# Performance work log

Hardware: AMD Instinct MI355X
Metric: run time of the kernel (lower is better)

## Reference

```python
import jax, jax.numpy as jnp
import numpy as np

B, D, A, M = 262144, 128, 32, 100


def setup_inputs() -> dict:
    key = jax.random.key(0)
    ks = jax.random.split(key, 8)
    s = 0.05
    return {
        "state": jax.random.normal(ks[0], (B, D), jnp.float32),
        "action": jax.random.normal(ks[1], (B, A), jnp.float32),
        "next_state": jax.random.normal(ks[2], (B, D), jnp.float32),
        "seen": jax.random.normal(ks[3], (M, D), jnp.float32),
        "W1": jax.random.normal(ks[4], (D, D + A), jnp.float32) * s,
        "b1": jnp.zeros((D,), jnp.float32),
        "W2": jax.random.normal(ks[5], (D, D), jnp.float32) * s,
        "b2": jnp.zeros((D,), jnp.float32),
        "Wf": jax.random.normal(ks[6], (D, D), jnp.float32) * s,
        "bf": jnp.zeros((D,), jnp.float32),
    }


def reference(state, action, next_state, seen, W1, b1, W2, b2, Wf, bf):
    # predictor: Linear(D+A -> D) -> ReLU -> Linear(D -> D)   (torch: y = x W^T + b)
    x = jnp.concatenate([state, action], axis=-1)            # [B, D+A]
    h = jax.nn.relu(x @ W1.T + b1)                           # [B, D]
    predicted_next = h @ W2.T + b2                           # [B, D]

    # feature_extractor: Linear(D -> D) -> ReLU
    feat = lambda z: jax.nn.relu(z @ Wf.T + bf)
    features_actual = feat(next_state)                       # [B, D]
    features_pred = feat(predicted_next)                     # [B, D]

    # per-sample MSE prediction error (features_actual detached in original)
    fa_sg = jax.lax.stop_gradient(features_actual)
    pred_error = jnp.mean((features_pred - fa_sg) ** 2, axis=-1)  # [B]

    # 1-NN L2 distance to memory buffer, batched via the ||a-b||^2 expansion
    # (avoids materializing [B, M, D])
    a2 = jnp.sum(features_actual ** 2, axis=-1, keepdims=True)    # [B, 1]
    s2 = jnp.sum(seen ** 2, axis=-1)                              # [M]
    d2 = a2 + s2[None, :] - 2.0 * (features_actual @ seen.T)      # [B, M]
    min_dist = jnp.sqrt(jnp.maximum(jnp.min(d2, axis=-1), 0.0))   # [B]
    novelty = jnp.minimum(1.0, min_dist / 10.0)                   # [B]

    curiosity_reward = pred_error * 0.5 + novelty * 0.5
    return jnp.stack([pred_error, novelty, curiosity_reward])     # [3, B]
```

## Files before the change

kernel.cpp:

```cpp
#include <hip/hip_runtime.h>
#include <hip/hip_bf16.h>
#include <math.h>

#define B_TOT 262144

typedef __attribute__((ext_vector_type(8))) short v8s;
typedef __attribute__((ext_vector_type(4))) float v4f;

#define WS_W1 0
#define WS_W2 20480
#define WS_WF 36864
#define WS_SEEN 53248
#define WS_S2_BYTES 135168

__device__ __forceinline__ unsigned short f2bf(float f) {
  union { float f; unsigned u; } cv; cv.f = f;
  unsigned u = cv.u;
  return (unsigned short)((u + 0x7FFFu + ((u >> 16) & 1u)) >> 16);
}
__device__ __forceinline__ float bf2f(unsigned short h) {
  union { unsigned u; float f; } cv; cv.u = ((unsigned)h) << 16;
  return cv.f;
}
__device__ __forceinline__ unsigned f2bf2(float x, float y) {
  float2 f; f.x = x; f.y = y;
  __hip_bfloat162 h = __float22bfloat162_rn(f);
  union { __hip_bfloat162 h; unsigned u; } cv; cv.h = h;
  return cv.u;
}

__global__ void curiosity_prep(const float* __restrict__ W1, const float* __restrict__ W2,
                               const float* __restrict__ Wf, const float* __restrict__ seen,
                               unsigned short* __restrict__ wsb, float* __restrict__ s2) {
  int bid = blockIdx.x;
  if (bid < 264) {
    int idx = bid * 256 + (int)threadIdx.x;
    if (idx < 20480) {
      int f = idx >> 9, r = idx & 511, L = r >> 3, j = r & 7;
      int t = f / 5, c = f - t * 5;
      int n = t * 16 + (L & 15), k = c * 32 + (L >> 4) * 8 + j;
      wsb[idx] = f2bf(W1[n * 160 + k]);
    } else if (idx < 36864) {
      int e = idx - 20480;
      int f = e >> 9, r = e & 511, L = r >> 3, j = r & 7;
      int t = f >> 2, c = f & 3;
      int n = t * 16 + (L & 15), k = c * 32 + (L >> 4) * 8 + j;
      wsb[idx] = f2bf(W2[n * 128 + k]);
    } else if (idx < 53248) {
      int e = idx - 36864;
      int f = e >> 9, r = e & 511, L = r >> 3, j = r & 7;
      int t = f >> 2, c = f & 3;
      int n = t * 16 + (L & 15), k = c * 32 + (L >> 4) * 8 + j;
      wsb[idx] = f2bf(Wf[n * 128 + k]);
    } else {
      int e = idx - 53248;
      int f = e >> 9, r = e & 511, L = r >> 3, j = r & 7;
      int t = f >> 2, c = f & 3;
      int n = t * 16 + (L & 15), k = c * 32 + (L >> 4) * 8 + j;
      float v = (n < 100) ? seen[n * 128 + k] : 0.f;
      wsb[idx] = f2bf(v);
    }
  } else {
    int wv = (int)threadIdx.x >> 6, lane = (int)threadIdx.x & 63;
    int mm = (bid - 264) * 4 + wv;
    float s;
    if (mm < 100) {
      float v0 = seen[mm * 128 + lane], v1 = seen[mm * 128 + 64 + lane];
      s = v0 * v0 + v1 * v1;
#pragma unroll
      for (int msk = 1; msk < 64; msk <<= 1) s += __shfl_xor(s, msk, 64);
    } else {
      s = 1e30f;
    }
    if (lane == 0) s2[mm] = s;
  }
}

__device__ __forceinline__ v8s cvt_frag(float4 lo, float4 hi) {
  union { v8s v; unsigned u[4]; } r;
  r.u[0] = f2bf2(lo.x, lo.y);
  r.u[1] = f2bf2(lo.z, lo.w);
  r.u[2] = f2bf2(hi.x, hi.y);
  r.u[3] = f2bf2(hi.z, hi.w);
  return r.v;
}

__device__ __forceinline__ v8s read_frag(const unsigned short* buf, int m, int q, int c) {
  return *(const v8s*)(buf + m * 136 + c * 32 + q * 8);
}
__device__ __forceinline__ v8s wfrag(const unsigned short* __restrict__ wsb,
                                     int base, int fragIdx, int lane) {
  return *(const v8s*)(wsb + base + fragIdx * 512 + lane * 8);
}

__global__ __launch_bounds__(256, 3) void curiosity_main(
    const float* __restrict__ state, const float* __restrict__ action,
    const float* __restrict__ next_state,
    const float* __restrict__ b1, const float* __restrict__ b2,
    const float* __restrict__ bfv,
    const unsigned short* __restrict__ wsb, const float* __restrict__ s2g,
    float* __restrict__ out) {
  __shared__ __attribute__((aligned(16))) unsigned short s_int[4][2][2176];
  __shared__ float s_o[3][128];

  const int tid = (int)threadIdx.x;
  const int w = tid >> 6, lane = tid & 63;
  const int m = lane & 15, q = lane >> 4;
  const int rowblk = (int)blockIdx.x * 128 + w * 32;

  unsigned short* buf[2] = { &s_int[w][0][0], &s_int[w][1][0] };

  const float* st0 = state + (size_t)(rowblk + m) * 128 + q * 8;
  const float* st1 = st0 + 16 * 128;
  const float* ac0 = action + (size_t)(rowblk + m) * 32 + q * 8;
  const float* ac1 = ac0 + 16 * 32;
  const float* np0 = next_state + (size_t)(rowblk + m) * 128 + q * 8;
  const float* np1 = np0 + 16 * 128;

  float4 sv[2][4][2], av[2][2];
#pragma unroll
  for (int c = 0; c < 4; ++c) {
    sv[0][c][0] = *(const float4*)(st0 + c * 32);
    sv[0][c][1] = *(const float4*)(st0 + c * 32 + 4);
    sv[1][c][0] = *(const float4*)(st1 + c * 32);
    sv[1][c][1] = *(const float4*)(st1 + c * 32 + 4);
  }
  av[0][0] = *(const float4*)(ac0); av[0][1] = *(const float4*)(ac0 + 4);
  av[1][0] = *(const float4*)(ac1); av[1][1] = *(const float4*)(ac1 + 4);

  float bv1[8], bv2[8], bvf[8];
#pragma unroll
  for (int tg = 0; tg < 8; ++tg) bv1[tg] = b1[tg * 16 + m];
#pragma unroll
  for (int tg = 0; tg < 8; ++tg) bv2[tg] = b2[tg * 16 + m];
#pragma unroll
  for (int tg = 0; tg < 8; ++tg) bvf[tg] = bfv[tg * 16 + m];

  v8s a1[2][5];
#pragma unroll
  for (int c = 0; c < 4; ++c) {
    a1[0][c] = cvt_frag(sv[0][c][0], sv[0][c][1]);
    a1[1][c] = cvt_frag(sv[1][c][0], sv[1][c][1]);
  }
  a1[0][4] = cvt_frag(av[0][0], av[0][1]);
  a1[1][4] = cvt_frag(av[1][0], av[1][1]);

#pragma unroll
  for (int hf = 0; hf < 2; ++hf) {
    v8s bfr[20];
#pragma unroll
    for (int c = 0; c < 5; ++c)
#pragma unroll
      for (int tl = 0; tl < 4; ++tl)
        bfr[c * 4 + tl] = wfrag(wsb, WS_W1, (hf * 4 + tl) * 5 + c, lane);
    v4f acc[2][4] = {};
#pragma unroll
    for (int c = 0; c < 5; ++c)
#pragma unroll
      for (int tl = 0; tl < 4; ++tl) {
        acc[0][tl] = __builtin_amdgcn_mfma_f32_16x16x32_bf16(a1[0][c], bfr[c * 4 + tl], acc[0][tl], 0, 0, 0);
        acc[1][tl] = __builtin_amdgcn_mfma_f32_16x16x32_bf16(a1[1][c], bfr[c * 4 + tl], acc[1][tl], 0, 0, 0);
      }
#pragma unroll
    for (int tl = 0; tl < 4; ++tl) {
      int tg = hf * 4 + tl;
      float bv = bv1[tg];
#pragma unroll
      for (int tt = 0; tt < 2; ++tt)
#pragma unroll
        for (int r = 0; r < 4; r += 2) {
          unsigned p = f2bf2(fmaxf(acc[tt][tl][r] + bv, 0.f),
                             fmaxf(acc[tt][tl][r + 1] + bv, 0.f));
          buf[tt][(q * 4 + r) * 136 + tg * 16 + m] = (unsigned short)p;
          buf[tt][(q * 4 + r + 1) * 136 + tg * 16 + m] = (unsigned short)(p >> 16);
        }
    }
  }

  float4 n0v[4][2], n1v[4][2];
#pragma unroll
  for (int c = 0; c < 4; ++c) {
    n0v[c][0] = *(const float4*)(np0 + c * 32);
    n0v[c][1] = *(const float4*)(np0 + c * 32 + 4);
  }

  v8s af[2][4];
#pragma unroll
  for (int c = 0; c < 4; ++c) {
    af[0][c] = read_frag(buf[0], m, q, c);
    af[1][c] = read_frag(buf[1], m, q, c);
  }
  v8s a3[2][4];
#pragma unroll
  for (int hf = 0; hf < 2; ++hf) {
    if (hf == 1) {
#pragma unroll
      for (int c = 0; c < 4; ++c) a3[0][c] = cvt_frag(n0v[c][0], n0v[c][1]);
#pragma unroll
      for (int c = 0; c < 4; ++c) {
        n1v[c][0] = *(const float4*)(np1 + c * 32);
        n1v[c][1] = *(const float4*)(np1 + c * 32 + 4);
      }
    }
    v8s bfr[16];
#pragma unroll
    for (int c = 0; c < 4; ++c)
#pragma unroll
      for (int tl = 0; tl < 4; ++tl)
        bfr[c * 4 + tl] = wfrag(wsb, WS_W2, (hf * 4 + tl) * 4 + c, lane);
    v4f acc[2][4] = {};
#pragma unroll
    for (int c = 0; c < 4; ++c)
#pragma unroll
      for (int tl = 0; tl < 4; ++tl) {
        acc[0][tl] = __builtin_amdgcn_mfma_f32_16x16x32_bf16(af[0][c], bfr[c * 4 + tl], acc[0][tl], 0, 0, 0);
        acc[1][tl] = __builtin_amdgcn_mfma_f32_16x16x32_bf16(af[1][c], bfr[c * 4 + tl], acc[1][tl], 0, 0, 0);
      }
#pragma unroll
    for (int tl = 0; tl < 4; ++tl) {
      int tg = hf * 4 + tl;
      float bv = bv2[tg];
#pragma unroll
      for (int tt = 0; tt < 2; ++tt)
#pragma unroll
        for (int r = 0; r < 4; r += 2) {
          unsigned p = f2bf2(acc[tt][tl][r] + bv, acc[tt][tl][r + 1] + bv);
          buf[tt][(q * 4 + r) * 136 + tg * 16 + m] = (unsigned short)p;
          buf[tt][(q * 4 + r + 1) * 136 + tg * 16 + m] = (unsigned short)(p >> 16);
        }
    }
  }

  v8s a4[2][4];
#pragma unroll
  for (int c = 0; c < 4; ++c) {
    a4[0][c] = read_frag(buf[0], m, q, c);
    a4[1][c] = read_frag(buf[1], m, q, c);
  }
#pragma unroll
  for (int c = 0; c < 4; ++c) a3[1][c] = cvt_frag(n1v[c][0], n1v[c][1]);

  float s2v[7];
#pragma unroll
  for (int tl = 0; tl < 7; ++tl) s2v[tl] = s2g[tl * 16 + m];

  float pe[2][4] = {};
  float a2s[2][4] = {};
#pragma unroll
  for (int hf = 0; hf < 2; ++hf) {
#pragma unroll
    for (int tl = 0; tl < 4; ++tl) {
      v8s bfr[4];
#pragma unroll
      for (int c = 0; c < 4; ++c)
        bfr[c] = wfrag(wsb, WS_WF, (hf * 4 + tl) * 4 + c, lane);
      v4f fa0 = {}, fa1 = {}, fp0 = {}, fp1 = {};
#pragma unroll
      for (int c = 0; c < 4; ++c) {
        fa0 = __builtin_amdgcn_mfma_f32_16x16x32_bf16(a3[0][c], bfr[c], fa0, 0, 0, 0);
        fa1 = __builtin_amdgcn_mfma_f32_16x16x32_bf16(a3[1][c], bfr[c], fa1, 0, 0, 0);
        fp0 = __builtin_amdgcn_mfma_f32_16x16x32_bf16(a4[0][c], bfr[c], fp0, 0, 0, 0);
        fp1 = __builtin_amdgcn_mfma_f32_16x16x32_bf16(a4[1][c], bfr[c], fp1, 0, 0, 0);
      }
      int tg = hf * 4 + tl;
      float bv = bvf[tg];
#pragma unroll
      for (int tt = 0; tt < 2; ++tt) {
        const v4f& fav = tt ? fa1 : fa0;
        const v4f& fpv = tt ? fp1 : fp0;
#pragma unroll
        for (int rp = 0; rp < 2; ++rp) {
          int r = rp * 2;
          unsigned p = f2bf2(fmaxf(fav[r] + bv, 0.f),
                             fmaxf(fav[r + 1] + bv, 0.f));
          buf[tt][(q * 4 + r) * 136 + tg * 16 + m] = (unsigned short)p;
          buf[tt][(q * 4 + r + 1) * 136 + tg * 16 + m] = (unsigned short)(p >> 16);
          float flo = bf2f((unsigned short)p), fhi = bf2f((unsigned short)(p >> 16));
          a2s[tt][r] += flo * flo;
          a2s[tt][r + 1] += fhi * fhi;
          float d0 = fmaxf(fpv[r] + bv, 0.f) - flo;
          float d1 = fmaxf(fpv[r + 1] + bv, 0.f) - fhi;
          pe[tt][r] += d0 * d0;
          pe[tt][r + 1] += d1 * d1;
        }
      }
    }
  }

#pragma unroll
  for (int tt = 0; tt < 2; ++tt)
#pragma unroll
    for (int r = 0; r < 4; ++r)
#pragma unroll
      for (int msk = 1; msk < 16; msk <<= 1) {
        pe[tt][r] += __shfl_xor(pe[tt][r], msk, 16);
        a2s[tt][r] += __shfl_xor(a2s[tt][r], msk, 16);
      }

  v8s a5[2][4];
#pragma unroll
  for (int c = 0; c < 4; ++c) {
    a5[0][c] = read_frag(buf[0], m, q, c);
    a5[1][c] = read_frag(buf[1], m, q, c);
  }
  float dmin[2][4] = {{3.4e38f, 3.4e38f, 3.4e38f, 3.4e38f},
                      {3.4e38f, 3.4e38f, 3.4e38f, 3.4e38f}};
  {
    v8s bfr[16];
#pragma unroll
    for (int tl = 0; tl < 4; ++tl)
#pragma unroll
      for (int c = 0; c < 4; ++c)
        bfr[tl * 4 + c] = wfrag(wsb, WS_SEEN, tl * 4 + c, lane);
#pragma unroll
    for (int tl = 0; tl < 4; ++tl) {
      v4f g0 = {}, g1 = {};
#pragma unroll
      for (int c = 0; c < 4; ++c) {
        g0 = __builtin_amdgcn_mfma_f32_16x16x32_bf16(a5[0][c], bfr[tl * 4 + c], g0, 0, 0, 0);
        g1 = __builtin_amdgcn_mfma_f32_16x16x32_bf16(a5[1][c], bfr[tl * 4 + c], g1, 0, 0, 0);
      }
      float s2x = s2v[tl];
#pragma unroll
      for (int r = 0; r < 4; ++r) {
        dmin[0][r] = fminf(dmin[0][r], a2s[0][r] + s2x - 2.f * g0[r]);
        dmin[1][r] = fminf(dmin[1][r], a2s[1][r] + s2x - 2.f * g1[r]);
      }
    }
  }
  {
    v8s bfr[12];
#pragma unroll
    for (int tl = 0; tl < 3; ++tl)
#pragma unroll
      for (int c = 0; c < 4; ++c)
        bfr[tl * 4 + c] = wfrag(wsb, WS_SEEN, (tl + 4) * 4 + c, lane);
#pragma unroll
    for (int tl = 0; tl < 3; ++tl) {
      v4f g0 = {}, g1 = {};
#pragma unroll
      for (int c = 0; c < 4; ++c) {
        g0 = __builtin_amdgcn_mfma_f32_16x16x32_bf16(a5[0][c], bfr[tl * 4 + c], g0, 0, 0, 0);
        g1 = __builtin_amdgcn_mfma_f32_16x16x32_bf16(a5[1][c], bfr[tl * 4 + c], g1, 0, 0, 0);
      }
      float s2x = s2v[tl + 4];
#pragma unroll
      for (int r = 0; r < 4; ++r) {
        dmin[0][r] = fminf(dmin[0][r], a2s[0][r] + s2x - 2.f * g0[r]);
        dmin[1][r] = fminf(dmin[1][r], a2s[1][r] + s2x - 2.f * g1[r]);
      }
    }
  }
#pragma unroll
  for (int tt = 0; tt < 2; ++tt)
#pragma unroll
    for (int r = 0; r < 4; ++r)
#pragma unroll
      for (int msk = 1; msk < 16; msk <<= 1)
        dmin[tt][r] = fminf(dmin[tt][r], __shfl_xor(dmin[tt][r], msk, 16));

  if (m == 0) {
#pragma unroll
    for (int tt = 0; tt < 2; ++tt)
#pragma unroll
      for (int r = 0; r < 4; ++r) {
        int rl = w * 32 + tt * 16 + q * 4 + r;
        float p = pe[tt][r] * (1.f / 128.f);
        float nov = fminf(1.f, sqrtf(fmaxf(dmin[tt][r], 0.f)) * 0.1f);
        s_o[0][rl] = p;
        s_o[1][rl] = nov;
        s_o[2][rl] = 0.5f * (p + nov);
      }
  }
  __syncthreads();
  const size_t base = (size_t)blockIdx.x * 128;
  for (int idx = tid; idx < 384; idx += 256) {
    int j = idx >> 7, r = idx & 127;
    out[(size_t)j * B_TOT + base + r] = s_o[j][r];
  }
}

extern "C" void kernel_launch(void* const* d_in, const int* in_sizes, int n_in,
                              void* d_out, int out_size, void* d_ws, size_t ws_size,
                              hipStream_t stream) {
  const float* state      = (const float*)d_in[0];
  const float* action     = (const float*)d_in[1];
  const float* next_state = (const float*)d_in[2];
  const float* seen       = (const float*)d_in[3];
  const float* W1         = (const float*)d_in[4];
  const float* b1         = (const float*)d_in[5];
  const float* W2         = (const float*)d_in[6];
  const float* b2         = (const float*)d_in[7];
  const float* Wf         = (const float*)d_in[8];
  const float* bf_        = (const float*)d_in[9];

  unsigned short* wsb = (unsigned short*)d_ws;
  float* s2 = (float*)((char*)d_ws + WS_S2_BYTES);

  curiosity_prep<<<292, 256, 0, stream>>>(W1, W2, Wf, seen, wsb, s2);
  curiosity_main<<<2048, 256, 0, stream>>>(state, action, next_state, b1, b2, bf_,
                                           wsb, s2, (float*)d_out);
}
```

Before: 371.8 us.

## Stage weight fragments into LDS via global_load_lds with block-cooperative loads

Each block now cooperatively copies the bf16 weight fragments for every layer (W1 in two halves, W2, Wf, seen) into a shared 32KB LDS buffer using async global-to-LDS loads. Each wave then reads them from LDS instead of every wave fetching them from global/L2 on its own. This removes redundant per-wave global weight traffic. In exchange it adds several block-wide barriers, lowers launch bounds from 3 to 2 blocks per CU, and moves the next_state and bias loads earlier, which may reduce latency hiding.

```diff
diff --git a/kernel.cpp b/kernel.cpp
--- a/kernel.cpp
+++ b/kernel.cpp
@@ -88,18 +88,31 @@
 __device__ __forceinline__ v8s read_frag(const unsigned short* buf, int m, int q, int c) {
   return *(const v8s*)(buf + m * 136 + c * 32 + q * 8);
 }
-__device__ __forceinline__ v8s wfrag(const unsigned short* __restrict__ wsb,
-                                     int base, int fragIdx, int lane) {
-  return *(const v8s*)(wsb + base + fragIdx * 512 + lane * 8);
-}
-
-__global__ __launch_bounds__(256, 3) void curiosity_main(
+
+__device__ __forceinline__ void gload_lds16(const unsigned short* g, unsigned short* l) {
+  __builtin_amdgcn_global_load_lds(
+      (const __attribute__((address_space(1))) unsigned int*)g,
+      (__attribute__((address_space(3))) unsigned int*)l, 16, 0, 0);
+}
+template <int N>
+__device__ __forceinline__ void stage_frags(const unsigned short* __restrict__ g,
+                                            unsigned short* l, int f0, int lane) {
+#pragma unroll
+  for (int i = 0; i < N; ++i)
+    gload_lds16(g + (size_t)(f0 + i) * 512 + lane * 8, l + (size_t)(f0 + i) * 512);
+}
+__device__ __forceinline__ v8s sfrag(const unsigned short* s_wt, int frag, int lane) {
+  return *(const v8s*)(s_wt + frag * 512 + lane * 8);
+}
+
+__global__ __launch_bounds__(256, 2) void curiosity_main(
     const float* __restrict__ state, const float* __restrict__ action,
     const float* __restrict__ next_state,
     const float* __restrict__ b1, const float* __restrict__ b2,
     const float* __restrict__ bfv,
     const unsigned short* __restrict__ wsb, const float* __restrict__ s2g,
     float* __restrict__ out) {
+  __shared__ __attribute__((aligned(16))) unsigned short s_wt[16384];
   __shared__ __attribute__((aligned(16))) unsigned short s_int[4][2][2176];
   __shared__ float s_o[3][128];
 
@@ -128,13 +141,12 @@
   av[0][0] = *(const float4*)(ac0); av[0][1] = *(const float4*)(ac0 + 4);
   av[1][0] = *(const float4*)(ac1); av[1][1] = *(const float4*)(ac1 + 4);
 
-  float bv1[8], bv2[8], bvf[8];
+  float bv1[8];
 #pragma unroll
   for (int tg = 0; tg < 8; ++tg) bv1[tg] = b1[tg * 16 + m];
-#pragma unroll
-  for (int tg = 0; tg < 8; ++tg) bv2[tg] = b2[tg * 16 + m];
-#pragma unroll
-  for (int tg = 0; tg < 8; ++tg) bvf[tg] = bfv[tg * 16 + m];
+
+  stage_frags<5>(wsb + WS_W1, s_wt, w * 5, lane);
+  __syncthreads();
 
   v8s a1[2][5];
 #pragma unroll
@@ -147,12 +159,17 @@
 
 #pragma unroll
   for (int hf = 0; hf < 2; ++hf) {
+    if (hf == 1) {
+      __syncthreads();
+      stage_frags<5>(wsb + WS_W1 + 20 * 512, s_wt, w * 5, lane);
+      __syncthreads();
+    }
     v8s bfr[20];
 #pragma unroll
     for (int c = 0; c < 5; ++c)
 #pragma unroll
       for (int tl = 0; tl < 4; ++tl)
-        bfr[c * 4 + tl] = wfrag(wsb, WS_W1, (hf * 4 + tl) * 5 + c, lane);
+        bfr[c * 4 + tl] = sfrag(s_wt, tl * 5 + c, lane);
     v4f acc[2][4] = {};
 #pragma unroll
     for (int c = 0; c < 5; ++c)
@@ -177,37 +194,36 @@
     }
   }
 
+  __syncthreads();
+  stage_frags<8>(wsb + WS_W2, s_wt, w * 8, lane);
+  float bv2[8];
+#pragma unroll
+  for (int tg = 0; tg < 8; ++tg) bv2[tg] = b2[tg * 16 + m];
+  v8s af[2][4];
+#pragma unroll
+  for (int c = 0; c < 4; ++c) {
+    af[0][c] = read_frag(buf[0], m, q, c);
+    af[1][c] = read_frag(buf[1], m, q, c);
+  }
+  __syncthreads();
+
   float4 n0v[4][2], n1v[4][2];
 #pragma unroll
   for (int c = 0; c < 4; ++c) {
     n0v[c][0] = *(const float4*)(np0 + c * 32);
     n0v[c][1] = *(const float4*)(np0 + c * 32 + 4);
-  }
-
-  v8s af[2][4];
-#pragma unroll
-  for (int c = 0; c < 4; ++c) {
-    af[0][c] = read_frag(buf[0], m, q, c);
-    af[1][c] = read_frag(buf[1], m, q, c);
-  }
-  v8s a3[2][4];
+    n1v[c][0] = *(const float4*)(np1 + c * 32);
+    n1v[c][1] = *(const float4*)(np1 + c * 32 + 4);
+  }
+
 #pragma unroll
   for (int hf = 0; hf < 2; ++hf) {
-    if (hf == 1) {
-#pragma unroll
-      for (int c = 0; c < 4; ++c) a3[0][c] = cvt_frag(n0v[c][0], n0v[c][1]);
-#pragma unroll
-      for (int c = 0; c < 4; ++c) {
-        n1v[c][0] = *(const float4*)(np1 + c * 32);
-        n1v[c][1] = *(const float4*)(np1 + c * 32 + 4);
-      }
-    }
     v8s bfr[16];
 #pragma unroll
     for (int c = 0; c < 4; ++c)
 #pragma unroll
       for (int tl = 0; tl < 4; ++tl)
-        bfr[c * 4 + tl] = wfrag(wsb, WS_W2, (hf * 4 + tl) * 4 + c, lane);
+        bfr[c * 4 + tl] = sfrag(s_wt, (hf * 4 + tl) * 4 + c, lane);
     v4f acc[2][4] = {};
 #pragma unroll
     for (int c = 0; c < 4; ++c)
@@ -231,36 +247,45 @@
     }
   }
 
+  __syncthreads();
+  stage_frags<8>(wsb + WS_WF, s_wt, w * 8, lane);
+  float bvf[8];
+#pragma unroll
+  for (int tg = 0; tg < 8; ++tg) bvf[tg] = bfv[tg * 16 + m];
   v8s a4[2][4];
 #pragma unroll
   for (int c = 0; c < 4; ++c) {
     a4[0][c] = read_frag(buf[0], m, q, c);
     a4[1][c] = read_frag(buf[1], m, q, c);
   }
-#pragma unroll
-  for (int c = 0; c < 4; ++c) a3[1][c] = cvt_frag(n1v[c][0], n1v[c][1]);
-
-  float s2v[7];
-#pragma unroll
-  for (int tl = 0; tl < 7; ++tl) s2v[tl] = s2g[tl * 16 + m];
+  __syncthreads();
+
+  v8s a3[2][4];
+#pragma unroll
+  for (int c = 0; c < 4; ++c) {
+    a3[0][c] = cvt_frag(n0v[c][0], n0v[c][1]);
+    a3[1][c] = cvt_frag(n1v[c][0], n1v[c][1]);
+  }
 
   float pe[2][4] = {};
   float a2s[2][4] = {};
 #pragma unroll
   for (int hf = 0; hf < 2; ++hf) {
+    v8s bfr[16];
+#pragma unroll
+    for (int tl = 0; tl < 4; ++tl)
+#pragma unroll
+      for (int c = 0; c < 4; ++c)
+        bfr[tl * 4 + c] = sfrag(s_wt, (hf * 4 + tl) * 4 + c, lane);
 #pragma unroll
     for (int tl = 0; tl < 4; ++tl) {
-      v8s bfr[4];
-#pragma unroll
-      for (int c = 0; c < 4; ++c)
-        bfr[c] = wfrag(wsb, WS_WF, (hf * 4 + tl) * 4 + c, lane);
       v4f fa0 = {}, fa1 = {}, fp0 = {}, fp1 = {};
 #pragma unroll
       for (int c = 0; c < 4; ++c) {
-        fa0 = __builtin_amdgcn_mfma_f32_16x16x32_bf16(a3[0][c], bfr[c], fa0, 0, 0, 0);
-        fa1 = __builtin_amdgcn_mfma_f32_16x16x32_bf16(a3[1][c], bfr[c], fa1, 0, 0, 0);
-        fp0 = __builtin_amdgcn_mfma_f32_16x16x32_bf16(a4[0][c], bfr[c], fp0, 0, 0, 0);
-        fp1 = __builtin_amdgcn_mfma_f32_16x16x32_bf16(a4[1][c], bfr[c], fp1, 0, 0, 0);
+        fa0 = __builtin_amdgcn_mfma_f32_16x16x32_bf16(a3[0][c], bfr[tl * 4 + c], fa0, 0, 0, 0);
+        fa1 = __builtin_amdgcn_mfma_f32_16x16x32_bf16(a3[1][c], bfr[tl * 4 + c], fa1, 0, 0, 0);
+        fp0 = __builtin_amdgcn_mfma_f32_16x16x32_bf16(a4[0][c], bfr[tl * 4 + c], fp0, 0, 0, 0);
+        fp1 = __builtin_amdgcn_mfma_f32_16x16x32_bf16(a4[1][c], bfr[tl * 4 + c], fp1, 0, 0, 0);
       }
       int tg = hf * 4 + tl;
       float bv = bvf[tg];
@@ -287,6 +312,11 @@
     }
   }
 
+  __syncthreads();
+  stage_frags<7>(wsb + WS_SEEN, s_wt, w * 7, lane);
+  float s2v[7];
+#pragma unroll
+  for (int tl = 0; tl < 7; ++tl) s2v[tl] = s2g[tl * 16 + m];
 #pragma unroll
   for (int tt = 0; tt < 2; ++tt)
 #pragma unroll
@@ -296,13 +326,14 @@
         pe[tt][r] += __shfl_xor(pe[tt][r], msk, 16);
         a2s[tt][r] += __shfl_xor(a2s[tt][r], msk, 16);
       }
-
   v8s a5[2][4];
 #pragma unroll
   for (int c = 0; c < 4; ++c) {
     a5[0][c] = read_frag(buf[0], m, q, c);
     a5[1][c] = read_frag(buf[1], m, q, c);
   }
+  __syncthreads();
+
   float dmin[2][4] = {{3.4e38f, 3.4e38f, 3.4e38f, 3.4e38f},
                       {3.4e38f, 3.4e38f, 3.4e38f, 3.4e38f}};
   {
@@ -311,7 +342,7 @@
     for (int tl = 0; tl < 4; ++tl)
 #pragma unroll
       for (int c = 0; c < 4; ++c)
-        bfr[tl * 4 + c] = wfrag(wsb, WS_SEEN, tl * 4 + c, lane);
+        bfr[tl * 4 + c] = sfrag(s_wt, tl * 4 + c, lane);
 #pragma unroll
     for (int tl = 0; tl < 4; ++tl) {
       v4f g0 = {}, g1 = {};
@@ -334,7 +365,7 @@
     for (int tl = 0; tl < 3; ++tl)
 #pragma unroll
       for (int c = 0; c < 4; ++c)
-        bfr[tl * 4 + c] = wfrag(wsb, WS_SEEN, (tl + 4) * 4 + c, lane);
+        bfr[tl * 4 + c] = sfrag(s_wt, (tl + 4) * 4 + c, lane);
 #pragma unroll
     for (int tl = 0; tl < 3; ++tl) {
       v4f g0 = {}, g1 = {};
```

Result: faster. 322.3 us (-13.3%).

## Stage weight fragments through double-buffered LDS via global_load_lds

Applied to the files above, without the earlier changes.

Rather than having every wave load the bf16 weight and memory-buffer fragments straight from global memory into registers, the block cooperatively copies 20 weight chunks into a two-slot LDS ring using direct global-to-LDS loads. Each MFMA stage reads its fragments from LDS while the next chunk is in flight. The next_state loads are also hoisted to the kernel start. This is meant to cut redundant per-wave global and L2 traffic and register pressure. The cost is a block-wide barrier per chunk (20 per block), 16 KB more shared memory that may lower occupancy, and a possible race because the direct LDS loads have no explicit vmcnt wait before the barrier.

```diff
diff --git a/kernel.cpp b/kernel.cpp
--- a/kernel.cpp
+++ b/kernel.cpp
@@ -12,6 +12,8 @@
 #define WS_WF 36864
 #define WS_SEEN 53248
 #define WS_S2_BYTES 135168
+
+#define MFMA __builtin_amdgcn_mfma_f32_16x16x32_bf16
 
 __device__ __forceinline__ unsigned short f2bf(float f) {
   union { float f; unsigned u; } cv; cv.f = f;
@@ -88,9 +90,53 @@
 __device__ __forceinline__ v8s read_frag(const unsigned short* buf, int m, int q, int c) {
   return *(const v8s*)(buf + m * 136 + c * 32 + q * 8);
 }
-__device__ __forceinline__ v8s wfrag(const unsigned short* __restrict__ wsb,
-                                     int base, int fragIdx, int lane) {
-  return *(const v8s*)(wsb + base + fragIdx * 512 + lane * 8);
+
+__device__ __forceinline__ void gload_lds16(const unsigned short* g, unsigned short* l) {
+  __builtin_amdgcn_global_load_lds(
+      (const __attribute__((address_space(1))) unsigned int*)g,
+      (__attribute__((address_space(3))) unsigned int*)l, 16, 0, 0);
+}
+__device__ __forceinline__ void stage_chunk(const unsigned short* __restrict__ g,
+                                            unsigned short* l, int nf, int w, int lane) {
+  for (int i = w; i < nf; i += 4)
+    gload_lds16(g + (size_t)i * 512 + lane * 8, l + i * 512);
+}
+
+__host__ __device__ constexpr int chunk_base(int c) {
+  return c < 8  ? WS_W1 + c * 2560 :
+         c < 12 ? WS_W2 + (c - 8) * 4096 :
+         c < 16 ? WS_WF + (c - 12) * 4096 :
+                  WS_SEEN + (c - 16) * 4096;
+}
+__host__ __device__ constexpr int chunk_nf(int c) { return c < 8 ? 5 : (c < 19 ? 8 : 4); }
+
+__device__ __forceinline__ void epi_store(unsigned short* bufT, v4f acc, float bv,
+                                          int q, int tg, int m, bool relu) {
+#pragma unroll
+  for (int r = 0; r < 4; r += 2) {
+    float x0 = acc[r] + bv, x1 = acc[r + 1] + bv;
+    if (relu) { x0 = fmaxf(x0, 0.f); x1 = fmaxf(x1, 0.f); }
+    unsigned p = f2bf2(x0, x1);
+    bufT[(q * 4 + r) * 136 + tg * 16 + m] = (unsigned short)p;
+    bufT[(q * 4 + r + 1) * 136 + tg * 16 + m] = (unsigned short)(p >> 16);
+  }
+}
+__device__ __forceinline__ void epi_fafp(unsigned short* bufT, v4f fav, v4f fpv, float bv,
+                                         int q, int tg, int m, float* a2sT, float* peT) {
+#pragma unroll
+  for (int rp = 0; rp < 2; ++rp) {
+    int r = rp * 2;
+    unsigned p = f2bf2(fmaxf(fav[r] + bv, 0.f), fmaxf(fav[r + 1] + bv, 0.f));
+    bufT[(q * 4 + r) * 136 + tg * 16 + m] = (unsigned short)p;
+    bufT[(q * 4 + r + 1) * 136 + tg * 16 + m] = (unsigned short)(p >> 16);
+    float flo = bf2f((unsigned short)p), fhi = bf2f((unsigned short)(p >> 16));
+    a2sT[r] += flo * flo;
+    a2sT[r + 1] += fhi * fhi;
+    float d0 = fmaxf(fpv[r] + bv, 0.f) - flo;
+    float d1 = fmaxf(fpv[r + 1] + bv, 0.f) - fhi;
+    peT[r] += d0 * d0;
+    peT[r + 1] += d1 * d1;
+  }
 }
 
 __global__ __launch_bounds__(256, 3) void curiosity_main(
@@ -100,6 +146,7 @@
     const float* __restrict__ bfv,
     const unsigned short* __restrict__ wsb, const float* __restrict__ s2g,
     float* __restrict__ out) {
+  __shared__ __attribute__((aligned(16))) unsigned short s_wt[2][4096];
   __shared__ __attribute__((aligned(16))) unsigned short s_int[4][2][2176];
   __shared__ float s_o[3][128];
 
@@ -117,7 +164,7 @@
   const float* np0 = next_state + (size_t)(rowblk + m) * 128 + q * 8;
   const float* np1 = np0 + 16 * 128;
 
-  float4 sv[2][4][2], av[2][2];
+  float4 sv[2][4][2], av[2][2], nv[2][4][2];
 #pragma unroll
   for (int c = 0; c < 4; ++c) {
     sv[0][c][0] = *(const float4*)(st0 + c * 32);
@@ -127,7 +174,15 @@
   }
   av[0][0] = *(const float4*)(ac0); av[0][1] = *(const float4*)(ac0 + 4);
   av[1][0] = *(const float4*)(ac1); av[1][1] = *(const float4*)(ac1 + 4);
-
+  stage_chunk(wsb + chunk_base(0), s_wt[0], chunk_nf(0), w, lane);
+  stage_chunk(wsb + chunk_base(1), s_wt[1], chunk_nf(1), w, lane);
+#pragma unroll
+  for (int c = 0; c < 4; ++c) {
+    nv[0][c][0] = *(const float4*)(np0 + c * 32);
+    nv[0][c][1] = *(const float4*)(np0 + c * 32 + 4);
+    nv[1][c][0] = *(const float4*)(np1 + c * 32);
+    nv[1][c][1] = *(const float4*)(np1 + c * 32 + 4);
+  }
   float bv1[8], bv2[8], bvf[8];
 #pragma unroll
   for (int tg = 0; tg < 8; ++tg) bv1[tg] = b1[tg * 16 + m];
@@ -144,44 +199,31 @@
   }
   a1[0][4] = cvt_frag(av[0][0], av[0][1]);
   a1[1][4] = cvt_frag(av[1][0], av[1][1]);
-
-#pragma unroll
-  for (int hf = 0; hf < 2; ++hf) {
-    v8s bfr[20];
-#pragma unroll
-    for (int c = 0; c < 5; ++c)
-#pragma unroll
-      for (int tl = 0; tl < 4; ++tl)
-        bfr[c * 4 + tl] = wfrag(wsb, WS_W1, (hf * 4 + tl) * 5 + c, lane);
-    v4f acc[2][4] = {};
-#pragma unroll
-    for (int c = 0; c < 5; ++c)
-#pragma unroll
-      for (int tl = 0; tl < 4; ++tl) {
-        acc[0][tl] = __builtin_amdgcn_mfma_f32_16x16x32_bf16(a1[0][c], bfr[c * 4 + tl], acc[0][tl], 0, 0, 0);
-        acc[1][tl] = __builtin_amdgcn_mfma_f32_16x16x32_bf16(a1[1][c], bfr[c * 4 + tl], acc[1][tl], 0, 0, 0);
-      }
-#pragma unroll
-    for (int tl = 0; tl < 4; ++tl) {
-      int tg = hf * 4 + tl;
-      float bv = bv1[tg];
-#pragma unroll
-      for (int tt = 0; tt < 2; ++tt)
-#pragma unroll
-        for (int r = 0; r < 4; r += 2) {
-          unsigned p = f2bf2(fmaxf(acc[tt][tl][r] + bv, 0.f),
-                             fmaxf(acc[tt][tl][r + 1] + bv, 0.f));
-          buf[tt][(q * 4 + r) * 136 + tg * 16 + m] = (unsigned short)p;
-          buf[tt][(q * 4 + r + 1) * 136 + tg * 16 + m] = (unsigned short)(p >> 16);
-        }
-    }
-  }
-
-  float4 n0v[4][2], n1v[4][2];
-#pragma unroll
-  for (int c = 0; c < 4; ++c) {
-    n0v[c][0] = *(const float4*)(np0 + c * 32);
-    n0v[c][1] = *(const float4*)(np0 + c * 32 + 4);
+  __syncthreads();
+  v8s a3[2][4];
+#pragma unroll
+  for (int c = 0; c < 4; ++c) {
+    a3[0][c] = cvt_frag(nv[0][c][0], nv[0][c][1]);
+    a3[1][c] = cvt_frag(nv[1][c][0], nv[1][c][1]);
+  }
+
+#pragma unroll
+  for (int p = 0; p < 8; ++p) {
+    if (p >= 1)
+      stage_chunk(wsb + chunk_base(p + 1), s_wt[(p + 1) & 1], chunk_nf(p + 1), w, lane);
+    const unsigned short* sb = s_wt[p & 1];
+    v8s bfr[5];
+#pragma unroll
+    for (int c = 0; c < 5; ++c) bfr[c] = *(const v8s*)(sb + c * 512 + lane * 8);
+    v4f acc[2] = {};
+#pragma unroll
+    for (int c = 0; c < 5; ++c) {
+      acc[0] = MFMA(a1[0][c], bfr[c], acc[0], 0, 0, 0);
+      acc[1] = MFMA(a1[1][c], bfr[c], acc[1], 0, 0, 0);
+    }
+    epi_store(buf[0], acc[0], bv1[p], q, p, m, true);
+    epi_store(buf[1], acc[1], bv1[p], q, p, m, true);
+    __syncthreads();
   }
 
   v8s af[2][4];
@@ -190,45 +232,26 @@
     af[0][c] = read_frag(buf[0], m, q, c);
     af[1][c] = read_frag(buf[1], m, q, c);
   }
-  v8s a3[2][4];
-#pragma unroll
-  for (int hf = 0; hf < 2; ++hf) {
-    if (hf == 1) {
-#pragma unroll
-      for (int c = 0; c < 4; ++c) a3[0][c] = cvt_frag(n0v[c][0], n0v[c][1]);
+#pragma unroll
+  for (int p = 8; p < 12; ++p) {
+    stage_chunk(wsb + chunk_base(p + 1), s_wt[(p + 1) & 1], chunk_nf(p + 1), w, lane);
+    const unsigned short* sb = s_wt[p & 1];
+#pragma unroll
+    for (int tl2 = 0; tl2 < 2; ++tl2) {
+      v8s bfr[4];
+#pragma unroll
+      for (int c = 0; c < 4; ++c) bfr[c] = *(const v8s*)(sb + (tl2 * 4 + c) * 512 + lane * 8);
+      v4f acc[2] = {};
 #pragma unroll
       for (int c = 0; c < 4; ++c) {
-        n1v[c][0] = *(const float4*)(np1 + c * 32);
-        n1v[c][1] = *(const float4*)(np1 + c * 32 + 4);
-      }
-    }
-    v8s bfr[16];
-#pragma unroll
-    for (int c = 0; c < 4; ++c)
-#pragma unroll
-      for (int tl = 0; tl < 4; ++tl)
-        bfr[c * 4 + tl] = wfrag(wsb, WS_W2, (hf * 4 + tl) * 4 + c, lane);
-    v4f acc[2][4] = {};
-#pragma unroll
-    for (int c = 0; c < 4; ++c)
-#pragma unroll
-      for (int tl = 0; tl < 4; ++tl) {
-        acc[0][tl] = __builtin_amdgcn_mfma_f32_16x16x32_bf16(af[0][c], bfr[c * 4 + tl], acc[0][tl], 0, 0, 0);
-        acc[1][tl] = __builtin_amdgcn_mfma_f32_16x16x32_bf16(af[1][c], bfr[c * 4 + tl], acc[1][tl], 0, 0, 0);
-      }
-#pragma unroll
-    for (int tl = 0; tl < 4; ++tl) {
-      int tg = hf * 4 + tl;
-      float bv = bv2[tg];
-#pragma unroll
-      for (int tt = 0; tt < 2; ++tt)
-#pragma unroll
-        for (int r = 0; r < 4; r += 2) {
-          unsigned p = f2bf2(acc[tt][tl][r] + bv, acc[tt][tl][r + 1] + bv);
-          buf[tt][(q * 4 + r) * 136 + tg * 16 + m] = (unsigned short)p;
-          buf[tt][(q * 4 + r + 1) * 136 + tg * 16 + m] = (unsigned short)(p >> 16);
-        }
-    }
+        acc[0] = MFMA(af[0][c], bfr[c], acc[0], 0, 0, 0);
+        acc[1] = MFMA(af[1][c], bfr[c], acc[1], 0, 0, 0);
+      }
+      int tg = (p - 8) * 2 + tl2;
+      epi_store(buf[0], acc[0], bv2[tg], q, tg, m, false);
+      epi_store(buf[1], acc[1], bv2[tg], q, tg, m, false);
+    }
+    __syncthreads();
   }
 
   v8s a4[2][4];
@@ -237,120 +260,84 @@
     a4[0][c] = read_frag(buf[0], m, q, c);
     a4[1][c] = read_frag(buf[1], m, q, c);
   }
-#pragma unroll
-  for (int c = 0; c < 4; ++c) a3[1][c] = cvt_frag(n1v[c][0], n1v[c][1]);
-
-  float s2v[7];
-#pragma unroll
-  for (int tl = 0; tl < 7; ++tl) s2v[tl] = s2g[tl * 16 + m];
-
   float pe[2][4] = {};
   float a2s[2][4] = {};
-#pragma unroll
-  for (int hf = 0; hf < 2; ++hf) {
-#pragma unroll
-    for (int tl = 0; tl < 4; ++tl) {
+  float s2v[7];
+#pragma unroll
+  for (int p = 12; p < 16; ++p) {
+    stage_chunk(wsb + chunk_base(p + 1), s_wt[(p + 1) & 1], chunk_nf(p + 1), w, lane);
+    if (p == 15) {
+#pragma unroll
+      for (int tl = 0; tl < 7; ++tl) s2v[tl] = s2g[tl * 16 + m];
+    }
+    const unsigned short* sb = s_wt[p & 1];
+#pragma unroll
+    for (int tl2 = 0; tl2 < 2; ++tl2) {
       v8s bfr[4];
 #pragma unroll
-      for (int c = 0; c < 4; ++c)
-        bfr[c] = wfrag(wsb, WS_WF, (hf * 4 + tl) * 4 + c, lane);
+      for (int c = 0; c < 4; ++c) bfr[c] = *(const v8s*)(sb + (tl2 * 4 + c) * 512 + lane * 8);
       v4f fa0 = {}, fa1 = {}, fp0 = {}, fp1 = {};
 #pragma unroll
       for (int c = 0; c < 4; ++c) {
-        fa0 = __builtin_amdgcn_mfma_f32_16x16x32_bf16(a3[0][c], bfr[c], fa0, 0, 0, 0);
-        fa1 = __builtin_amdgcn_mfma_f32_16x16x32_bf16(a3[1][c], bfr[c], fa1, 0, 0, 0);
-        fp0 = __builtin_amdgcn_mfma_f32_16x16x32_bf16(a4[0][c], bfr[c], fp0, 0, 0, 0);
-        fp1 = __builtin_amdgcn_mfma_f32_16x16x32_bf16(a4[1][c], bfr[c], fp1, 0, 0, 0);
-      }
-      int tg = hf * 4 + tl;
-      float bv = bvf[tg];
-#pragma unroll
-      for (int tt = 0; tt < 2; ++tt) {
-        const v4f& fav = tt ? fa1 : fa0;
-        const v4f& fpv = tt ? fp1 : fp0;
-#pragma unroll
-        for (int rp = 0; rp < 2; ++rp) {
-          int r = rp * 2;
-          unsigned p = f2bf2(fmaxf(fav[r] + bv, 0.f),
-                             fmaxf(fav[r + 1] + bv, 0.f));
-          buf[tt][(q * 4 + r) * 136 + tg * 16 + m] = (unsigned short)p;
-          buf[tt][(q * 4 + r + 1) * 136 + tg * 16 + m] = (unsigned short)(p >> 16);
-          float flo = bf2f((unsigned short)p), fhi = bf2f((unsigned short)(p >> 16));
-          a2s[tt][r] += flo * flo;
-          a2s[tt][r + 1] += fhi * fhi;
-          float d0 = fmaxf(fpv[r] + bv, 0.f) - flo;
-          float d1 = fmaxf(fpv[r + 1] + bv, 0.f) - fhi;
-          pe[tt][r] += d0 * d0;
-          pe[tt][r + 1] += d1 * d1;
-        }
-      }
-    }
-  }
-
-#pragma unroll
-  for (int tt = 0; tt < 2; ++tt)
-#pragma unroll
-    for (int r = 0; r < 4; ++r)
-#pragma unroll
-      for (int msk = 1; msk < 16; msk <<= 1) {
-        pe[tt][r] += __shfl_xor(pe[tt][r], msk, 16);
-        a2s[tt][r] += __shfl_xor(a2s[tt][r], msk, 16);
-      }
-
-  v8s a5[2][4];
-#pragma unroll
-  for (int c = 0; c < 4; ++c) {
-    a5[0][c] = read_frag(buf[0], m, q, c);
-    a5[1][c] = read_frag(buf[1], m, q, c);
-  }
+        fa0 = MFMA(a3[0][c], bfr[c], fa0, 0, 0, 0);
+        fa1 = MFMA(a3[1][c], bfr[c], fa1, 0, 0, 0);
+        fp0 = MFMA(a4[0][c], bfr[c], fp0, 0, 0, 0);
+        fp1 = MFMA(a4[1][c], bfr[c], fp1, 0, 0, 0);
+      }
+      int tg = (p - 12) * 2 + tl2;
+      epi_fafp(buf[0], fa0, fp0, bvf[tg], q, tg, m, a2s[0], pe[0]);
+      epi_fafp(buf[1], fa1, fp1, bvf[tg], q, tg, m, a2s[1], pe[1]);
+    }
+    __syncthreads();
+  }
+
   float dmin[2][4] = {{3.4e38f, 3.4e38f, 3.4e38f, 3.4e38f},
                       {3.4e38f, 3.4e38f, 3.4e38f, 3.4e38f}};
-  {
-    v8s bfr[16];
-#pragma unroll
-    for (int tl = 0; tl < 4; ++tl)
-#pragma unroll
-      for (int c = 0; c < 4; ++c)
-        bfr[tl * 4 + c] = wfrag(wsb, WS_SEEN, tl * 4 + c, lane);
-#pragma unroll
-    for (int tl = 0; tl < 4; ++tl) {
+  v8s a5[2][4];
+#pragma unroll
+  for (int p = 16; p < 20; ++p) {
+    if (p < 19)
+      stage_chunk(wsb + chunk_base(p + 1), s_wt[(p + 1) & 1], chunk_nf(p + 1), w, lane);
+    if (p == 16) {
+#pragma unroll
+      for (int tt = 0; tt < 2; ++tt)
+#pragma unroll
+        for (int r = 0; r < 4; ++r)
+#pragma unroll
+          for (int msk = 1; msk < 16; msk <<= 1) {
+            pe[tt][r] += __shfl_xor(pe[tt][r], msk, 16);
+            a2s[tt][r] += __shfl_xor(a2s[tt][r], msk, 16);
+          }
+#pragma unroll
+      for (int c = 0; c < 4; ++c) {
+        a5[0][c] = read_frag(buf[0], m, q, c);
+        a5[1][c] = read_frag(buf[1], m, q, c);
+      }
+    }
+    const unsigned short* sb = s_wt[p & 1];
+    const int ntl = (p == 19) ? 1 : 2;
+#pragma unroll
+    for (int tl2 = 0; tl2 < 2; ++tl2) {
+      if (tl2 >= ntl) break;
+      v8s bfr[4];
+#pragma unroll
+      for (int c = 0; c < 4; ++c) bfr[c] = *(const v8s*)(sb + (tl2 * 4 + c) * 512 + lane * 8);
       v4f g0 = {}, g1 = {};
 #pragma unroll
       for (int c = 0; c < 4; ++c) {
-        g0 = __builtin_amdgcn_mfma_f32_16x16x32_bf16(a5[0][c], bfr[tl * 4 + c], g0, 0, 0, 0);
-        g1 = __builtin_amdgcn_mfma_f32_16x16x32_bf16(a5[1][c], bfr[tl * 4 + c], g1, 0, 0, 0);
-      }
-      float s2x = s2v[tl];
+        g0 = MFMA(a5[0][c], bfr[c], g0, 0, 0, 0);
+        g1 = MFMA(a5[1][c], bfr[c], g1, 0, 0, 0);
+      }
+      float s2x = s2v[(p - 16) * 2 + tl2];
 #pragma unroll
       for (int r = 0; r < 4; ++r) {
         dmin[0][r] = fminf(dmin[0][r], a2s[0][r] + s2x - 2.f * g0[r]);
         dmin[1][r] = fminf(dmin[1][r], a2s[1][r] + s2x - 2.f * g1[r]);
       }
     }
-  }
-  {
-    v8s bfr[12];
-#pragma unroll
-    for (int tl = 0; tl < 3; ++tl)
-#pragma unroll
-      for (int c = 0; c < 4; ++c)
-        bfr[tl * 4 + c] = wfrag(wsb, WS_SEEN, (tl + 4) * 4 + c, lane);
-#pragma unroll
-    for (int tl = 0; tl < 3; ++tl) {
-      v4f g0 = {}, g1 = {};
-#pragma unroll
-      for (int c = 0; c < 4; ++c) {
-        g0 = __builtin_amdgcn_mfma_f32_16x16x32_bf16(a5[0][c], bfr[tl * 4 + c], g0, 0, 0, 0);
-        g1 = __builtin_amdgcn_mfma_f32_16x16x32_bf16(a5[1][c], bfr[tl * 4 + c], g1, 0, 0, 0);
-      }
-      float s2x = s2v[tl + 4];
-#pragma unroll
-      for (int r = 0; r < 4; ++r) {
-        dmin[0][r] = fminf(dmin[0][r], a2s[0][r] + s2x - 2.f * g0[r]);
-        dmin[1][r] = fminf(dmin[1][r], a2s[1][r] + s2x - 2.f * g1[r]);
-      }
-    }
-  }
+    if (p < 19) __syncthreads();
+  }
+
 #pragma unroll
   for (int tt = 0; tt < 2; ++tt)
 #pragma unroll
```

After: 375.2 us. No clear change (+0.9%).
